# Optimization experiments

Measured on AMD Instinct MI355X. Metric: run time of the kernel, lower is better.

The kernel has to match this reference:

```python
import jax, jax.numpy as jnp
import numpy as np

N = 100000      # nodes
E = 1600000     # edges
G = 256         # graphs in the batch
D_IN = 128
H = 128
C = 10
EPS = 1e-5      # BatchNorm eps


def setup_inputs() -> dict:
    key = jax.random.key(0)
    ks = jax.random.split(key, 32)
    inp = {
        'x': jax.random.normal(ks[0], (N, D_IN), jnp.float32),
        'edge_index': jax.random.randint(ks[1], (2, E), 0, N, dtype=jnp.int64),
        'batch': jnp.sort(jax.random.randint(ks[2], (N,), 0, G, dtype=jnp.int64)),
        'w1': jax.random.normal(ks[3], (D_IN, H), jnp.float32) * 0.05,
        'b1': jax.random.normal(ks[4], (H,), jnp.float32) * 0.05,
        'w2': jax.random.normal(ks[5], (H, H), jnp.float32) * 0.05,
        'b2': jax.random.normal(ks[6], (H,), jnp.float32) * 0.05,
        'w3': jax.random.normal(ks[7], (H, H), jnp.float32) * 0.05,
        'b3': jax.random.normal(ks[8], (H,), jnp.float32) * 0.05,
        'g1': jax.random.uniform(ks[9], (H,), jnp.float32, 0.5, 1.5),
        'be1': jax.random.normal(ks[10], (H,), jnp.float32) * 0.05,
        'm1': jax.random.normal(ks[11], (H,), jnp.float32) * 0.05,
        'v1': jax.random.uniform(ks[12], (H,), jnp.float32, 0.5, 1.5),
        'g2': jax.random.uniform(ks[13], (H,), jnp.float32, 0.5, 1.5),
        'be2': jax.random.normal(ks[14], (H,), jnp.float32) * 0.05,
        'm2': jax.random.normal(ks[15], (H,), jnp.float32) * 0.05,
        'v2': jax.random.uniform(ks[16], (H,), jnp.float32, 0.5, 1.5),
        'g3': jax.random.uniform(ks[17], (H,), jnp.float32, 0.5, 1.5),
        'be3': jax.random.normal(ks[18], (H,), jnp.float32) * 0.05,
        'm3': jax.random.normal(ks[19], (H,), jnp.float32) * 0.05,
        'v3': jax.random.uniform(ks[20], (H,), jnp.float32, 0.5, 1.5),
        'fcw1': jax.random.normal(ks[21], (H, H // 2), jnp.float32) * 0.05,
        'fcb1': jax.random.normal(ks[22], (H // 2,), jnp.float32) * 0.05,
        'fcw2': jax.random.normal(ks[23], (H // 2, C), jnp.float32) * 0.05,
        'fcb2': jax.random.normal(ks[24], (C,), jnp.float32) * 0.05,
    }
    return inp


def _gcn_norm(edge_index, n_nodes):
    # add self loops (PyG GCNConv default) and compute D^-1/2 (A+I) D^-1/2 norms
    loop = jnp.arange(n_nodes, dtype=edge_index.dtype)
    src = jnp.concatenate([edge_index[0], loop])
    dst = jnp.concatenate([edge_index[1], loop])
    deg = jax.ops.segment_sum(jnp.ones_like(dst, dtype=jnp.float32), dst, num_segments=n_nodes)
    dinv = jnp.where(deg > 0, jax.lax.rsqrt(deg), 0.0)
    norm = dinv[src] * dinv[dst]  # [E+N]
    return src, dst, norm


def _gcn_conv(x, W, b, src, dst, norm, n_nodes):
    h = x @ W                                   # [N, H]
    msg = norm[:, None] * h[src]                # gather + scale, [E+N, H]
    return jax.ops.segment_sum(msg, dst, num_segments=n_nodes) + b


def _bn_eval(x, gamma, beta, mean, var):
    return (x - mean) * jax.lax.rsqrt(var + EPS) * gamma + beta


def reference(x, edge_index, batch, w1, b1, w2, b2, w3, b3,
              g1, be1, m1, v1, g2, be2, m2, v2, g3, be3, m3, v3,
              fcw1, fcb1, fcw2, fcb2):
    n = x.shape[0]
    x = jnp.nan_to_num(x, nan=0.0, posinf=1e6, neginf=-1e6)
    src, dst, norm = _gcn_norm(edge_index, n)

    h = jax.nn.relu(_bn_eval(_gcn_conv(x, w1, b1, src, dst, norm, n), g1, be1, m1, v1))
    h = jax.nn.relu(_bn_eval(_gcn_conv(h, w2, b2, src, dst, norm, n), g2, be2, m2, v2))
    h = jax.nn.relu(_bn_eval(_gcn_conv(h, w3, b3, src, dst, norm, n), g3, be3, m3, v3))

    # global_mean_pool over graphs
    sums = jax.ops.segment_sum(h, batch, num_segments=G)            # [G, H]
    cnts = jax.ops.segment_sum(jnp.ones((n,), h.dtype), batch, num_segments=G)
    pooled = sums / jnp.maximum(cnts, 1.0)[:, None]

    out = jax.nn.relu(pooled @ fcw1 + fcb1) @ fcw2 + fcb2           # [G, C]
    return out
```

## Files before the change

### kernel.cpp

```cpp
#include <hip/hip_runtime.h>
#include <math.h>

#define NN 100000
#define EE 1600000
#define GG 256
#define HH 128
#define BSH 8
#define NBK 391
#define PASSA_WG 391
#define CAPB 6144

typedef __attribute__((ext_vector_type(8))) short short8;
typedef __attribute__((ext_vector_type(4))) float f32x4;
typedef __attribute__((ext_vector_type(2))) float f32x2;

union U4S8 { uint4 u; short8 s; };

static __device__ __forceinline__ unsigned bf16rne(float f) {
    const unsigned u = __float_as_uint(f);
    return (u + 0x7fffu + ((u >> 16) & 1u)) >> 16;
}
static __device__ __forceinline__ unsigned packbf(float a, float b) {
    return bf16rne(a) | (bf16rne(b) << 16);
}
static __device__ __forceinline__ float bflo(unsigned u) { return __uint_as_float(u << 16); }
static __device__ __forceinline__ float bfhi(unsigned u) { return __uint_as_float(u & 0xffff0000u); }
static __device__ __forceinline__ f32x2 up2(unsigned u) {
    f32x2 r; r.x = bflo(u); r.y = bfhi(u); return r;
}

__global__ __launch_bounds__(256) void setup_k(
    const int* __restrict__ ei, const int* __restrict__ batch,
    const float* __restrict__ w1, const float* __restrict__ w2,
    const float* __restrict__ w3,
    const float* __restrict__ b1, const float* __restrict__ g1,
    const float* __restrict__ be1, const float* __restrict__ m1,
    const float* __restrict__ v1,
    const float* __restrict__ b2, const float* __restrict__ g2,
    const float* __restrict__ be2, const float* __restrict__ m2,
    const float* __restrict__ v2,
    const float* __restrict__ b3, const float* __restrict__ g3,
    const float* __restrict__ be3, const float* __restrict__ m3,
    const float* __restrict__ v3,
    unsigned* __restrict__ bt, float* __restrict__ sc, float* __restrict__ sh,
    int* __restrict__ cursor, float* __restrict__ psum, int* __restrict__ gcnt,
    int* __restrict__ flags) {
    const int id = blockIdx.x * 256 + threadIdx.x;
    if (id < 24576) {
        const int w = id >> 13;
        const int rem = id & 8191;
        const int n = rem >> 6;
        const int kk = rem & 63;
        const float* W = (w == 0) ? w1 : (w == 1) ? w2 : w3;
        bt[id] = packbf(W[(2 * kk) * HH + n], W[(2 * kk + 1) * HH + n]);
    } else if (id < 24704) {
        const int c = id - 24576;
        float s;
        s = g1[c] / sqrtf(v1[c] + 1e-5f);
        sc[c] = s;           sh[c] = (b1[c] - m1[c]) * s + be1[c];
        s = g2[c] / sqrtf(v2[c] + 1e-5f);
        sc[128 + c] = s;     sh[128 + c] = (b2[c] - m2[c]) * s + be2[c];
        s = g3[c] / sqrtf(v3[c] + 1e-5f);
        sc[256 + c] = s;     sh[256 + c] = (b3[c] - m3[c]) * s + be3[c];
    } else if (id < 25095) {
        const int b = id - 24704;
        cursor[b] = b * CAPB;
    } else if (id < 57863) {
        psum[id - 25095] = 0.0f;
    } else if (id < 58119) {
        gcnt[id - 57863] = 0;
    } else if (id == 58119) {
        int e64 = 1;
        for (int j = 0; j < 8; ++j) {
            if (ei[2 * EE - 1 - 2 * j] != 0) { e64 = 0; break; }
        }
        flags[0] = e64;
        flags[1] = (batch[NN - 1] == 0) ? 1 : 0;
    }
}
#define SETUP_GRID 228

__global__ __launch_bounds__(256) void passA_k(const int* __restrict__ ei,
                                               const int* __restrict__ flags,
                                               int* __restrict__ cursor,
                                               unsigned* __restrict__ pairs) {
    __shared__ int h[NBK];
    __shared__ int rbase[NBK];
    const int tid = threadIdx.x;
    for (int i = tid; i < NBK; i += 256) h[i] = 0;
    __syncthreads();
    const bool e64 = flags[0] != 0;
    const int base = blockIdx.x * 4096;
    int scache[16], dcache[16];
#pragma unroll
    for (int j = 0; j < 16; ++j) {
        const int e = base + j * 256 + tid;
        int s = -1, d = 0;
        if (e < EE) {
            s = e64 ? ei[2 * e] : ei[e];
            d = e64 ? ei[2 * (EE + e)] : ei[EE + e];
            atomicAdd(&h[d >> BSH], 1);
        }
        scache[j] = s; dcache[j] = d;
    }
    __syncthreads();
    for (int i = tid; i < NBK; i += 256) {
        const int c = h[i];
        rbase[i] = c ? atomicAdd(&cursor[i], c) : 0;
    }
    __syncthreads();
    for (int i = tid; i < NBK; i += 256) h[i] = 0;
    __syncthreads();
#pragma unroll
    for (int j = 0; j < 16; ++j) {
        const int s = scache[j];
        if (s >= 0) {
            const int d = dcache[j];
            const int b = d >> BSH;
            const int r = atomicAdd(&h[b], 1);
            pairs[rbase[b] + r] = ((unsigned)(d & 255) << 17) | (unsigned)s;
        }
    }
}

__global__ __launch_bounds__(256) void passB_k(const unsigned* __restrict__ pairs,
                                               const int* __restrict__ cursor,
                                               int* __restrict__ offs,
                                               int* __restrict__ degcnt,
                                               float* __restrict__ dinv,
                                               int* __restrict__ csr) {
    __shared__ unsigned pk[CAPB];
    __shared__ int lcs[CAPB];
    __shared__ int cnt[256];
    __shared__ int loff[256];
    __shared__ int sc[256];
    __shared__ int tot;
    const int tid = threadIdx.x;
    const int b = blockIdx.x;
    const int p0 = b * CAPB;
    const int np = cursor[b] - p0;
    const int nb0 = b << BSH;
    const int nnode = (NN - nb0 < 256) ? (NN - nb0) : 256;

    cnt[tid] = 0;
    __syncthreads();
    for (int i = tid; i < np; i += 256) {
        const unsigned p = pairs[p0 + i];
        pk[i] = p;
        atomicAdd(&cnt[p >> 17], 1);
    }
    __syncthreads();
    const int creal = cnt[tid];
    const int cpad = (tid < nnode) ? ((creal + 8) & ~7) : 0;
    sc[tid] = cpad;
    __syncthreads();
    for (int off = 1; off < 256; off <<= 1) {
        int t = (tid >= off) ? sc[tid - off] : 0;
        __syncthreads();
        sc[tid] += t;
        __syncthreads();
    }
    const int ex = sc[tid] - cpad;
    loff[tid] = ex;
    if (tid == 255) tot = sc[255];
    if (tid < nnode) {
        const int node = nb0 + tid;
        offs[node] = p0 + ex;
        degcnt[node] = creal;
        dinv[node] = 1.0f / sqrtf((float)(creal + 1));
    }
    __syncthreads();
    cnt[tid] = 0;
    __syncthreads();
    for (int i = tid; i < np; i += 256) {
        const unsigned p = pk[i];
        const int dl = (int)(p >> 17);
        const int r = atomicAdd(&cnt[dl], 1);
        lcs[loff[dl] + r] = (int)(p & 0x1FFFFu);
    }
    __syncthreads();
    if (tid < nnode) {
        const int b0 = loff[tid];
        for (int j = 1; j < creal; ++j) {
            const int key = lcs[b0 + j];
            int k2 = j - 1;
            while (k2 >= 0 && lcs[b0 + k2] > key) {
                lcs[b0 + k2 + 1] = lcs[b0 + k2];
                --k2;
            }
            lcs[b0 + k2 + 1] = key;
        }
        lcs[b0 + creal] = nb0 + tid;
        for (int j = creal + 1; j < cpad; ++j) lcs[b0 + j] = NN;
    }
    __syncthreads();
    for (int i = tid; i < tot; i += 256) csr[p0 + i] = lcs[i];
}

static __device__ __forceinline__ float sani(float v) {
    if (isnan(v)) return 0.0f;
    if (isinf(v)) return v > 0.0f ? 1e6f : -1e6f;
    return v;
}

__global__ __launch_bounds__(256) void gemm_mfma_k(const float* __restrict__ Af,
                                                   const unsigned* __restrict__ btg,
                                                   const float* __restrict__ dinv,
                                                   unsigned* __restrict__ C, int M) {
    __shared__ unsigned lds_u[8704];
    const int tid = threadIdx.x;
    const int wave = tid >> 6;
    const int lane = tid & 63;
    const int nl = lane & 15;
    const int q = lane >> 4;
    const int row0 = blockIdx.x * 64 + wave * 16;
    const int rowg = row0 + nl;
    const int rowa = min(rowg, M - 1);

    {
        const uint4* __restrict__ bg4 = (const uint4*)btg;
        for (int i = tid; i < 2048; i += 256) {
            const int n = i >> 4, w4 = i & 15;
            *(uint4*)&lds_u[n * 68 + w4 * 4] = bg4[n * 16 + w4];
        }
    }

    short8 a[4];
#pragma unroll
    for (int ks = 0; ks < 4; ++ks) {
        const float4 p = *(const float4*)(Af + (size_t)rowa * HH + ks * 32 + q * 8);
        const float4 r = *(const float4*)(Af + (size_t)rowa * HH + ks * 32 + q * 8 + 4);
        U4S8 cv;
        cv.u = make_uint4(packbf(sani(p.x), sani(p.y)), packbf(sani(p.z), sani(p.w)),
                          packbf(sani(r.x), sani(r.y)), packbf(sani(r.z), sani(r.w)));
        a[ks] = cv.s;
    }

    __syncthreads();

    f32x4 acc[8];
#pragma unroll
    for (int t = 0; t < 8; ++t) acc[t] = (f32x4)0.0f;

    const unsigned short* __restrict__ bts = (const unsigned short*)lds_u;
#pragma unroll
    for (int ks = 0; ks < 4; ++ks) {
#pragma unroll
        for (int t = 0; t < 8; ++t) {
            const int n = t * 16 + nl;
            const short8 b = *(const short8*)(bts + n * 136 + ks * 32 + q * 8);
            acc[t] = __builtin_amdgcn_mfma_f32_16x16x32_bf16(b, a[ks], acc[t], 0, 0, 0);
        }
    }

    if (rowg < M) {
        const float dsc = dinv[rowg];
        unsigned* crow = C + (size_t)rowg * 64;
#pragma unroll
        for (int t = 0; t < 8; ++t) {
            uint2 o;
            o.x = packbf(dsc * acc[t][0], dsc * acc[t][1]);
            o.y = packbf(dsc * acc[t][2], dsc * acc[t][3]);
            *(uint2*)(crow + t * 8 + q * 2) = o;
        }
    } else if (rowg == M) {
        unsigned* crow = C + (size_t)M * 64;
#pragma unroll
        for (int t = 0; t < 8; ++t)
            *(uint2*)(crow + t * 8 + q * 2) = make_uint2(0u, 0u);
    }
}

static __device__ __forceinline__ void gather4(
    const char* __restrict__ hb, const int* __restrict__ csr,
    const int st[4], const int np[4], const int maxp,
    const int sub, const unsigned cgo, f32x2 acc[4][4]) {
    int ia[4], ib[4];
#pragma unroll
    for (int i = 0; i < 4; ++i) {
        ia[i] = csr[st[i] + sub];
        ib[i] = csr[st[i] + 4 + sub];
    }
    for (int e = 0; e < maxp; e += 8) {
        uint4 r[8];
#pragma unroll
        for (int i = 0; i < 4; ++i) {
            const bool act = (e < np[i]);
            const unsigned sA = act ? (unsigned)ia[i] : (unsigned)NN;
            const unsigned sB = act ? (unsigned)ib[i] : (unsigned)NN;
            r[2 * i]     = *(const uint4*)(hb + ((sA << 8) | cgo));
            r[2 * i + 1] = *(const uint4*)(hb + ((sB << 8) | cgo));
        }
#pragma unroll
        for (int i = 0; i < 4; ++i) {
            ia[i] = csr[st[i] + e + 8 + sub];
            ib[i] = csr[st[i] + e + 12 + sub];
        }
#pragma unroll
        for (int i = 0; i < 4; ++i) {
            const uint4 rA = r[2 * i];
            const uint4 rB = r[2 * i + 1];
            acc[i][0] += up2(rA.x) + up2(rB.x);
            acc[i][1] += up2(rA.y) + up2(rB.y);
            acc[i][2] += up2(rA.z) + up2(rB.z);
            acc[i][3] += up2(rA.w) + up2(rB.w);
        }
    }
}

__global__ __launch_bounds__(256) void agg_gemm_k(
    const unsigned* __restrict__ hin, const int* __restrict__ csr,
    const int* __restrict__ offs, const int* __restrict__ cnt,
    const float* __restrict__ dinv,
    const float* __restrict__ bnsc, const float* __restrict__ bnsh,
    const unsigned* __restrict__ btg,
    unsigned* __restrict__ hout) {
    __shared__ unsigned ybuf[16 * 68];
    const int tid = threadIdx.x;
    const int wave = tid >> 6;
    const int lane = tid & 63;
    const int cg = lane & 15;
    const int sub = lane >> 4;
    const int c8 = cg * 8;
    const char* __restrict__ hb = (const char*)hin;
    const unsigned cgo = (unsigned)(cg << 4);

    if (blockIdx.x == 0 && tid < 64) hout[(size_t)NN * 64 + tid] = 0u;

    int st[4], np[4];
    float dvv[4];
#pragma unroll
    for (int i = 0; i < 4; ++i) {
        const int v = __builtin_amdgcn_readfirstlane(blockIdx.x * 16 + wave * 4 + i);
        st[i] = offs[v];
        np[i] = (cnt[v] + 8) & ~7;
        dvv[i] = dinv[v];
    }
    const int maxp = max(max(np[0], np[1]), max(np[2], np[3]));

    f32x2 acc[4][4];
#pragma unroll
    for (int i = 0; i < 4; ++i)
#pragma unroll
        for (int j = 0; j < 4; ++j) acc[i][j] = (f32x2)0.0f;

    gather4(hb, csr, st, np, maxp, sub, cgo, acc);

    const float4 sca = *(const float4*)(bnsc + c8);
    const float4 scb = *(const float4*)(bnsc + c8 + 4);
    const float4 sha = *(const float4*)(bnsh + c8);
    const float4 shb = *(const float4*)(bnsh + c8 + 4);

#pragma unroll
    for (int i = 0; i < 4; ++i) {
#pragma unroll
        for (int j = 0; j < 4; ++j) {
            acc[i][j].x += __shfl_xor(acc[i][j].x, 16);
            acc[i][j].y += __shfl_xor(acc[i][j].y, 16);
            acc[i][j].x += __shfl_xor(acc[i][j].x, 32);
            acc[i][j].y += __shfl_xor(acc[i][j].y, 32);
        }
        if (sub == 0) {
            const float dv = dvv[i];
            const float y0 = fmaxf(dv * acc[i][0].x * sca.x + sha.x, 0.0f);
            const float y1 = fmaxf(dv * acc[i][0].y * sca.y + sha.y, 0.0f);
            const float y2 = fmaxf(dv * acc[i][1].x * sca.z + sha.z, 0.0f);
            const float y3 = fmaxf(dv * acc[i][1].y * sca.w + sha.w, 0.0f);
            const float y4 = fmaxf(dv * acc[i][2].x * scb.x + shb.x, 0.0f);
            const float y5 = fmaxf(dv * acc[i][2].y * scb.y + shb.y, 0.0f);
            const float y6 = fmaxf(dv * acc[i][3].x * scb.z + shb.z, 0.0f);
            const float y7 = fmaxf(dv * acc[i][3].y * scb.w + shb.w, 0.0f);
            *(uint4*)&ybuf[(wave * 4 + i) * 68 + cg * 4] =
                make_uint4(packbf(y0, y1), packbf(y2, y3), packbf(y4, y5), packbf(y6, y7));
        }
    }
    __syncthreads();

    const int nl = cg;
    const int q = sub;
    short8 arow[4];
#pragma unroll
    for (int ks = 0; ks < 4; ++ks) {
        U4S8 cv;
        cv.u = *(const uint4*)&ybuf[nl * 68 + ks * 16 + q * 4];
        arow[ks] = cv.s;
    }
    const uint4* __restrict__ bt4 = (const uint4*)btg;
    const int t0 = wave * 2;
    f32x4 acc0 = (f32x4)0.0f, acc1 = (f32x4)0.0f;
#pragma unroll
    for (int ks = 0; ks < 4; ++ks) {
        U4S8 b0, b1;
        b0.u = bt4[((t0 + 0) * 16 + nl) * 16 + ks * 4 + q];
        b1.u = bt4[((t0 + 1) * 16 + nl) * 16 + ks * 4 + q];
        acc0 = __builtin_amdgcn_mfma_f32_16x16x32_bf16(b0.s, arow[ks], acc0, 0, 0, 0);
        acc1 = __builtin_amdgcn_mfma_f32_16x16x32_bf16(b1.s, arow[ks], acc1, 0, 0, 0);
    }
    const int rowg = blockIdx.x * 16 + nl;
    const float dsc = dinv[rowg];
    unsigned* crow = hout + (size_t)rowg * 64;
    uint2 o0, o1;
    o0.x = packbf(dsc * acc0[0], dsc * acc0[1]);
    o0.y = packbf(dsc * acc0[2], dsc * acc0[3]);
    o1.x = packbf(dsc * acc1[0], dsc * acc1[1]);
    o1.y = packbf(dsc * acc1[2], dsc * acc1[3]);
    *(uint2*)(crow + (t0 + 0) * 8 + q * 2) = o0;
    *(uint2*)(crow + (t0 + 1) * 8 + q * 2) = o1;
}

__global__ __launch_bounds__(256) void agg_pool_k(
    const unsigned* __restrict__ hpre, const int* __restrict__ csr,
    const int* __restrict__ offs, const int* __restrict__ cnt,
    const float* __restrict__ dinv,
    const float* __restrict__ bnsc, const float* __restrict__ bnsh,
    const int* __restrict__ batch, const int* __restrict__ flags,
    float* __restrict__ psum, int* __restrict__ gcnt) {
    __shared__ float yb[16][128];
    __shared__ int gid[16];
    const int tid = threadIdx.x;
    const int wave = tid >> 6;
    const int lane = tid & 63;
    const int cg = lane & 15;
    const int sub = lane >> 4;
    const int c8 = cg * 8;
    const char* __restrict__ hb = (const char*)hpre;
    const unsigned cgo = (unsigned)(cg << 4);
    const bool b64 = flags[1] != 0;

    int st[4], np[4];
    float dvv[4];
#pragma unroll
    for (int i = 0; i < 4; ++i) {
        const int v = __builtin_amdgcn_readfirstlane(blockIdx.x * 16 + wave * 4 + i);
        st[i] = offs[v];
        np[i] = (cnt[v] + 8) & ~7;
        dvv[i] = dinv[v];
        if (lane == 0) gid[wave * 4 + i] = b64 ? batch[2 * v] : batch[v];
    }
    const int maxp = max(max(np[0], np[1]), max(np[2], np[3]));

    f32x2 acc[4][4];
#pragma unroll
    for (int i = 0; i < 4; ++i)
#pragma unroll
        for (int j = 0; j < 4; ++j) acc[i][j] = (f32x2)0.0f;

    gather4(hb, csr, st, np, maxp, sub, cgo, acc);

    const float4 sca = *(const float4*)(bnsc + c8);
    const float4 scb = *(const float4*)(bnsc + c8 + 4);
    const float4 sha = *(const float4*)(bnsh + c8);
    const float4 shb = *(const float4*)(bnsh + c8 + 4);

#pragma unroll
    for (int i = 0; i < 4; ++i) {
#pragma unroll
        for (int j = 0; j < 4; ++j) {
            acc[i][j].x += __shfl_xor(acc[i][j].x, 16);
            acc[i][j].y += __shfl_xor(acc[i][j].y, 16);
            acc[i][j].x += __shfl_xor(acc[i][j].x, 32);
            acc[i][j].y += __shfl_xor(acc[i][j].y, 32);
        }
        if (sub == 0) {
            const float dv = dvv[i];
            const int row = wave * 4 + i;
            yb[row][c8 + 0] = fmaxf(dv * acc[i][0].x * sca.x + sha.x, 0.0f);
            yb[row][c8 + 1] = fmaxf(dv * acc[i][0].y * sca.y + sha.y, 0.0f);
            yb[row][c8 + 2] = fmaxf(dv * acc[i][1].x * sca.z + sha.z, 0.0f);
            yb[row][c8 + 3] = fmaxf(dv * acc[i][1].y * sca.w + sha.w, 0.0f);
            yb[row][c8 + 4] = fmaxf(dv * acc[i][2].x * scb.x + shb.x, 0.0f);
            yb[row][c8 + 5] = fmaxf(dv * acc[i][2].y * scb.y + shb.y, 0.0f);
            yb[row][c8 + 6] = fmaxf(dv * acc[i][3].x * scb.z + shb.z, 0.0f);
            yb[row][c8 + 7] = fmaxf(dv * acc[i][3].y * scb.w + shb.w, 0.0f);
        }
    }
    __syncthreads();

    if (tid < 128) {
        float s = 0.0f;
        int cur = gid[0];
        for (int r = 0; r < 16; ++r) {
            const int g = gid[r];
            if (g != cur) {
                atomicAdd(&psum[cur * HH + tid], s);
                cur = g; s = 0.0f;
            }
            s += yb[r][tid];
        }
        atomicAdd(&psum[cur * HH + tid], s);
    } else if (tid == 128) {
        int cur = gid[0], c = 0;
        for (int r = 0; r < 16; ++r) {
            const int g = gid[r];
            if (g != cur) {
                atomicAdd(&gcnt[cur], c);
                cur = g; c = 0;
            }
            ++c;
        }
        atomicAdd(&gcnt[cur], c);
    }
}

__global__ __launch_bounds__(128) void head_k(
    const float* __restrict__ psum, const int* __restrict__ gcnt,
    const float* __restrict__ fw1, const float* __restrict__ fb1,
    const float* __restrict__ fw2, const float* __restrict__ fb2,
    float* __restrict__ out) {
    __shared__ float pooled[128];
    __shared__ float hid[64];
    const int g = blockIdx.x;
    const int tid = threadIdx.x;

    const int cntn = gcnt[g];
    pooled[tid] = psum[g * HH + tid] / (float)(cntn > 0 ? cntn : 1);
    __syncthreads();

    if (tid < 64) {
        float a = fb1[tid];
#pragma unroll 4
        for (int k = 0; k < 128; ++k) a += pooled[k] * fw1[k * 64 + tid];
        hid[tid] = fmaxf(a, 0.0f);
    }
    __syncthreads();
    if (tid < 10) {
        float a = fb2[tid];
#pragma unroll
        for (int k = 0; k < 64; ++k) a += hid[k] * fw2[k * 10 + tid];
        out[g * 10 + tid] = a;
    }
}

extern "C" void kernel_launch(void* const* d_in, const int* in_sizes, int n_in,
                              void* d_out, int out_size, void* d_ws, size_t ws_size,
                              hipStream_t stream) {
    const float* x_in  = (const float*)d_in[0];
    const int*   ei    = (const int*)d_in[1];
    const int*   batch = (const int*)d_in[2];
    const float* w1 = (const float*)d_in[3];
    const float* b1 = (const float*)d_in[4];
    const float* w2 = (const float*)d_in[5];
    const float* b2 = (const float*)d_in[6];
    const float* w3 = (const float*)d_in[7];
    const float* b3 = (const float*)d_in[8];
    const float* g1 = (const float*)d_in[9];
    const float* be1 = (const float*)d_in[10];
    const float* m1 = (const float*)d_in[11];
    const float* v1 = (const float*)d_in[12];
    const float* g2 = (const float*)d_in[13];
    const float* be2 = (const float*)d_in[14];
    const float* m2 = (const float*)d_in[15];
    const float* v2 = (const float*)d_in[16];
    const float* g3 = (const float*)d_in[17];
    const float* be3 = (const float*)d_in[18];
    const float* m3 = (const float*)d_in[19];
    const float* v3 = (const float*)d_in[20];
    const float* fw1 = (const float*)d_in[21];
    const float* fb1 = (const float*)d_in[22];
    const float* fw2 = (const float*)d_in[23];
    const float* fb2 = (const float*)d_in[24];
    float* out = (float*)d_out;

    size_t off = 0;
    char* base = (char*)d_ws;
    auto alloc = [&](size_t bytes) -> void* {
        void* p = base + off;
        off += (bytes + 255) & ~(size_t)255;
        return p;
    };
    int*      degcnt = (int*)alloc((size_t)NN * 4);
    float*    dinv   = (float*)alloc((size_t)NN * 4);
    int*      offs   = (int*)alloc((size_t)NN * 4);
    int*      cursor = (int*)alloc((size_t)NBK * 4);
    int*      flags  = (int*)alloc(256);
    float*    bnsc   = (float*)alloc(3 * 128 * 4);
    float*    bnsh   = (float*)alloc(3 * 128 * 4);
    unsigned* btg    = (unsigned*)alloc(3 * 8192 * 4);
    float*    psum   = (float*)alloc((size_t)GG * HH * 4);
    int*      gcnt   = (int*)alloc((size_t)GG * 4);
    int*      csr    = (int*)alloc((size_t)NBK * CAPB * 4);
    unsigned* pairs  = (unsigned*)alloc((size_t)NBK * CAPB * 4);
    unsigned* bufA   = (unsigned*)alloc((size_t)(NN + 1) * 64 * 4);
    unsigned* bufB   = (unsigned*)alloc((size_t)(NN + 1) * 64 * 4);
    if (off > ws_size) return;

    setup_k<<<SETUP_GRID, 256, 0, stream>>>(ei, batch, w1, w2, w3,
                                            b1, g1, be1, m1, v1,
                                            b2, g2, be2, m2, v2,
                                            b3, g3, be3, m3, v3,
                                            btg, bnsc, bnsh, cursor, psum, gcnt,
                                            flags);
    passA_k<<<PASSA_WG, 256, 0, stream>>>(ei, flags, cursor, pairs);
    passB_k<<<NBK, 256, 0, stream>>>(pairs, cursor, offs, degcnt, dinv, csr);

    const int ggrid = (NN + 63) / 64;
    const int fgrid = NN / 16;

    gemm_mfma_k<<<ggrid, 256, 0, stream>>>(x_in, btg, dinv, bufA, NN);
    agg_gemm_k<<<fgrid, 256, 0, stream>>>(bufA, csr, offs, degcnt, dinv,
                                          bnsc, bnsh, btg + 8192, bufB);
    agg_gemm_k<<<fgrid, 256, 0, stream>>>(bufB, csr, offs, degcnt, dinv,
                                          bnsc + 128, bnsh + 128, btg + 16384, bufA);
    agg_pool_k<<<fgrid, 256, 0, stream>>>(bufA, csr, offs, degcnt, dinv,
                                          bnsc + 256, bnsh + 256, batch, flags,
                                          psum, gcnt);
    head_k<<<GG, 128, 0, stream>>>(psum, gcnt, fw1, fb1, fw2, fb2, out);
}
```

Measured before the change: 448.4 us.

## Store layer-2 input features in fp8 and drop per-node CSR sort

The first aggregation kernel now writes its output as fp8 (128 bytes per row instead of 256), and the second aggregation gathers fp8 rows and unpacks them with hardware conversion builtins. This halves the random-gather traffic for one of the three message-passing layers. Separately, passB no longer insertion-sorts each node's neighbour list in LDS and writes the scattered CSR entries straight to global memory, which removes the serial per-thread sort and an LDS staging copy. The costs are reduced numerical precision in the layer-2 features and a non-deterministic neighbour order, which changes the floating-point summation order.

```diff
diff --git a/kernel.cpp b/kernel.cpp
--- a/kernel.cpp
+++ b/kernel.cpp
@@ -130,11 +130,9 @@
                                                float* __restrict__ dinv,
                                                int* __restrict__ csr) {
     __shared__ unsigned pk[CAPB];
-    __shared__ int lcs[CAPB];
     __shared__ int cnt[256];
     __shared__ int loff[256];
     __shared__ int sc[256];
-    __shared__ int tot;
     const int tid = threadIdx.x;
     const int b = blockIdx.x;
     const int p0 = b * CAPB;
@@ -162,7 +160,6 @@
     }
     const int ex = sc[tid] - cpad;
     loff[tid] = ex;
-    if (tid == 255) tot = sc[255];
     if (tid < nnode) {
         const int node = nb0 + tid;
         offs[node] = p0 + ex;
@@ -176,25 +173,13 @@
         const unsigned p = pk[i];
         const int dl = (int)(p >> 17);
         const int r = atomicAdd(&cnt[dl], 1);
-        lcs[loff[dl] + r] = (int)(p & 0x1FFFFu);
-    }
-    __syncthreads();
+        csr[p0 + loff[dl] + r] = (int)(p & 0x1FFFFu);
+    }
     if (tid < nnode) {
-        const int b0 = loff[tid];
-        for (int j = 1; j < creal; ++j) {
-            const int key = lcs[b0 + j];
-            int k2 = j - 1;
-            while (k2 >= 0 && lcs[b0 + k2] > key) {
-                lcs[b0 + k2 + 1] = lcs[b0 + k2];
-                --k2;
-            }
-            lcs[b0 + k2 + 1] = key;
-        }
-        lcs[b0 + creal] = nb0 + tid;
-        for (int j = creal + 1; j < cpad; ++j) lcs[b0 + j] = NN;
-    }
-    __syncthreads();
-    for (int i = tid; i < tot; i += 256) csr[p0 + i] = lcs[i];
+        const int basep = p0 + loff[tid];
+        csr[basep + creal] = nb0 + tid;
+        for (int j = creal + 1; j < cpad; ++j) csr[basep + j] = NN;
+    }
 }
 
 static __device__ __forceinline__ float sani(float v) {
@@ -271,7 +256,7 @@
     }
 }
 
-static __device__ __forceinline__ void gather4(
+static __device__ __forceinline__ void gather4_bf16(
     const char* __restrict__ hb, const int* __restrict__ csr,
     const int st[4], const int np[4], const int maxp,
     const int sub, const unsigned cgo, f32x2 acc[4][4]) {
@@ -308,7 +293,49 @@
     }
 }
 
-__global__ __launch_bounds__(256) void agg_gemm_k(
+static __device__ __forceinline__ void gather4_fp8(
+    const char* __restrict__ hb, const int* __restrict__ csr,
+    const int st[4], const int np[4], const int maxp,
+    const int sub, const unsigned cgo8, f32x2 acc[4][4]) {
+    int ia[4], ib[4];
+#pragma unroll
+    for (int i = 0; i < 4; ++i) {
+        ia[i] = csr[st[i] + sub];
+        ib[i] = csr[st[i] + 4 + sub];
+    }
+    for (int e = 0; e < maxp; e += 8) {
+        uint2 r[8];
+#pragma unroll
+        for (int i = 0; i < 4; ++i) {
+            const bool act = (e < np[i]);
+            const unsigned sA = act ? (unsigned)ia[i] : (unsigned)NN;
+            const unsigned sB = act ? (unsigned)ib[i] : (unsigned)NN;
+            r[2 * i]     = *(const uint2*)(hb + ((sA << 7) | cgo8));
+            r[2 * i + 1] = *(const uint2*)(hb + ((sB << 7) | cgo8));
+        }
+#pragma unroll
+        for (int i = 0; i < 4; ++i) {
+            ia[i] = csr[st[i] + e + 8 + sub];
+            ib[i] = csr[st[i] + e + 12 + sub];
+        }
+#pragma unroll
+        for (int i = 0; i < 4; ++i) {
+            const uint2 rA = r[2 * i];
+            const uint2 rB = r[2 * i + 1];
+            acc[i][0] += __builtin_amdgcn_cvt_pk_f32_fp8(rA.x, false)
+                       + __builtin_amdgcn_cvt_pk_f32_fp8(rB.x, false);
+            acc[i][1] += __builtin_amdgcn_cvt_pk_f32_fp8(rA.x, true)
+                       + __builtin_amdgcn_cvt_pk_f32_fp8(rB.x, true);
+            acc[i][2] += __builtin_amdgcn_cvt_pk_f32_fp8(rA.y, false)
+                       + __builtin_amdgcn_cvt_pk_f32_fp8(rB.y, false);
+            acc[i][3] += __builtin_amdgcn_cvt_pk_f32_fp8(rA.y, true)
+                       + __builtin_amdgcn_cvt_pk_f32_fp8(rB.y, true);
+        }
+    }
+}
+
+template <int IN8, int OUT8>
+__global__ __launch_bounds__(256) void agg_gemm_t(
     const unsigned* __restrict__ hin, const int* __restrict__ csr,
     const int* __restrict__ offs, const int* __restrict__ cnt,
     const float* __restrict__ dinv,
@@ -323,9 +350,11 @@
     const int sub = lane >> 4;
     const int c8 = cg * 8;
     const char* __restrict__ hb = (const char*)hin;
-    const unsigned cgo = (unsigned)(cg << 4);
-
-    if (blockIdx.x == 0 && tid < 64) hout[(size_t)NN * 64 + tid] = 0u;
+
+    if (blockIdx.x == 0) {
+        if (OUT8) { if (tid < 32) hout[(size_t)NN * 32 + tid] = 0u; }
+        else      { if (tid < 64) hout[(size_t)NN * 64 + tid] = 0u; }
+    }
 
     int st[4], np[4];
     float dvv[4];
@@ -344,7 +373,8 @@
 #pragma unroll
         for (int j = 0; j < 4; ++j) acc[i][j] = (f32x2)0.0f;
 
-    gather4(hb, csr, st, np, maxp, sub, cgo, acc);
+    if (IN8) gather4_fp8(hb, csr, st, np, maxp, sub, (unsigned)(cg << 3), acc);
+    else     gather4_bf16(hb, csr, st, np, maxp, sub, (unsigned)(cg << 4), acc);
 
     const float4 sca = *(const float4*)(bnsc + c8);
     const float4 scb = *(const float4*)(bnsc + c8 + 4);
@@ -398,14 +428,25 @@
     }
     const int rowg = blockIdx.x * 16 + nl;
     const float dsc = dinv[rowg];
-    unsigned* crow = hout + (size_t)rowg * 64;
-    uint2 o0, o1;
-    o0.x = packbf(dsc * acc0[0], dsc * acc0[1]);
-    o0.y = packbf(dsc * acc0[2], dsc * acc0[3]);
-    o1.x = packbf(dsc * acc1[0], dsc * acc1[1]);
-    o1.y = packbf(dsc * acc1[2], dsc * acc1[3]);
-    *(uint2*)(crow + (t0 + 0) * 8 + q * 2) = o0;
-    *(uint2*)(crow + (t0 + 1) * 8 + q * 2) = o1;
+    if (OUT8) {
+        char* crow = (char*)hout + (size_t)rowg * 128;
+        unsigned u0 = 0, u1 = 0;
+        u0 = __builtin_amdgcn_cvt_pk_fp8_f32(dsc * acc0[0], dsc * acc0[1], u0, false);
+        u0 = __builtin_amdgcn_cvt_pk_fp8_f32(dsc * acc0[2], dsc * acc0[3], u0, true);
+        u1 = __builtin_amdgcn_cvt_pk_fp8_f32(dsc * acc1[0], dsc * acc1[1], u1, false);
+        u1 = __builtin_amdgcn_cvt_pk_fp8_f32(dsc * acc1[2], dsc * acc1[3], u1, true);
+        *(unsigned*)(crow + (t0 + 0) * 16 + q * 4) = u0;
+        *(unsigned*)(crow + (t0 + 1) * 16 + q * 4) = u1;
+    } else {
+        unsigned* crow = hout + (size_t)rowg * 64;
+        uint2 o0, o1;
+        o0.x = packbf(dsc * acc0[0], dsc * acc0[1]);
+        o0.y = packbf(dsc * acc0[2], dsc * acc0[3]);
+        o1.x = packbf(dsc * acc1[0], dsc * acc1[1]);
+        o1.y = packbf(dsc * acc1[2], dsc * acc1[3]);
+        *(uint2*)(crow + (t0 + 0) * 8 + q * 2) = o0;
+        *(uint2*)(crow + (t0 + 1) * 8 + q * 2) = o1;
+    }
 }
 
 __global__ __launch_bounds__(256) void agg_pool_k(
@@ -445,7 +486,7 @@
 #pragma unroll
         for (int j = 0; j < 4; ++j) acc[i][j] = (f32x2)0.0f;
 
-    gather4(hb, csr, st, np, maxp, sub, cgo, acc);
+    gather4_bf16(hb, csr, st, np, maxp, sub, cgo, acc);
 
     const float4 sca = *(const float4*)(bnsc + c8);
     const float4 scb = *(const float4*)(bnsc + c8 + 4);
@@ -581,7 +622,7 @@
     int*      csr    = (int*)alloc((size_t)NBK * CAPB * 4);
     unsigned* pairs  = (unsigned*)alloc((size_t)NBK * CAPB * 4);
     unsigned* bufA   = (unsigned*)alloc((size_t)(NN + 1) * 64 * 4);
-    unsigned* bufB   = (unsigned*)alloc((size_t)(NN + 1) * 64 * 4);
+    unsigned* bufB   = (unsigned*)alloc((size_t)(NN + 1) * 32 * 4);
     if (off > ws_size) return;
 
     setup_k<<<SETUP_GRID, 256, 0, stream>>>(ei, batch, w1, w2, w3,
@@ -597,10 +638,10 @@
     const int fgrid = NN / 16;
 
     gemm_mfma_k<<<ggrid, 256, 0, stream>>>(x_in, btg, dinv, bufA, NN);
-    agg_gemm_k<<<fgrid, 256, 0, stream>>>(bufA, csr, offs, degcnt, dinv,
-                                          bnsc, bnsh, btg + 8192, bufB);
-    agg_gemm_k<<<fgrid, 256, 0, stream>>>(bufB, csr, offs, degcnt, dinv,
-                                          bnsc + 128, bnsh + 128, btg + 16384, bufA);
+    agg_gemm_t<0, 1><<<fgrid, 256, 0, stream>>>(bufA, csr, offs, degcnt, dinv,
+                                                bnsc, bnsh, btg + 8192, bufB);
+    agg_gemm_t<1, 0><<<fgrid, 256, 0, stream>>>(bufB, csr, offs, degcnt, dinv,
+                                                bnsc + 128, bnsh + 128, btg + 16384, bufA);
     agg_pool_k<<<fgrid, 256, 0, stream>>>(bufA, csr, offs, degcnt, dinv,
                                           bnsc + 256, bnsh + 256, batch, flags,
                                           psum, gcnt);
```

Result: faster. 402.4 us (-10.2%).
